# Kernel optimization log

Hardware: AMD Instinct MI355X
Metric: run time of the kernel (lower is better)

The kernel has to match this reference:

```python
import jax, jax.numpy as jnp
import numpy as np

D_MODEL = 2048
NUM_HEADS = 16
HEAD_DIM = D_MODEL // NUM_HEADS
D_FF = 4 * D_MODEL
B, L = 2, 2048
LN_EPS = 1e-6


def layer_norm(x, scale, bias):
    x32 = x.astype(jnp.float32)
    mu = jnp.mean(x32, axis=-1, keepdims=True)
    var = jnp.mean(jnp.square(x32 - mu), axis=-1, keepdims=True)
    return (x32 - mu) * jax.lax.rsqrt(var + LN_EPS) * scale + bias


def setup_inputs() -> dict:
    key = jax.random.key(0)
    ks = jax.random.split(key, 10)
    s = 1.0 / np.sqrt(D_MODEL)
    x = jax.random.normal(ks[0], (B, L, D_MODEL), dtype=jnp.float32)
    mask = jnp.tril(jnp.ones((L, L), dtype=bool))[None, None, :, :]  # causal [1,1,L,L]
    wq = jax.random.normal(ks[1], (D_MODEL, D_MODEL), jnp.float32) * s
    wk = jax.random.normal(ks[2], (D_MODEL, D_MODEL), jnp.float32) * s
    wv = jax.random.normal(ks[3], (D_MODEL, D_MODEL), jnp.float32) * s
    wo = jax.random.normal(ks[4], (D_MODEL, D_MODEL), jnp.float32) * s
    w1 = jax.random.normal(ks[5], (D_MODEL, D_FF), jnp.float32) * s
    b1 = jnp.zeros((D_FF,), jnp.float32)
    w2 = jax.random.normal(ks[6], (D_FF, D_MODEL), jnp.float32) * (1.0 / np.sqrt(D_FF))
    b2 = jnp.zeros((D_MODEL,), jnp.float32)
    ln1_scale = jnp.ones((D_MODEL,), jnp.float32)
    ln1_bias = jnp.zeros((D_MODEL,), jnp.float32)
    ln2_scale = jnp.ones((D_MODEL,), jnp.float32)
    ln2_bias = jnp.zeros((D_MODEL,), jnp.float32)
    return {"x": x, "mask": mask, "ln1_scale": ln1_scale, "ln1_bias": ln1_bias,
            "wq": wq, "wk": wk, "wv": wv, "wo": wo,
            "ln2_scale": ln2_scale, "ln2_bias": ln2_bias,
            "w1": w1, "b1": b1, "w2": w2, "b2": b2}


def reference(x, mask, ln1_scale, ln1_bias, wq, wk, wv, wo,
              ln2_scale, ln2_bias, w1, b1, w2, b2):
    residual = x
    h = layer_norm(x, ln1_scale, ln1_bias)
    b, l, _ = h.shape
    q = (h @ wq).reshape(b, l, NUM_HEADS, HEAD_DIM)
    k = (h @ wk).reshape(b, l, NUM_HEADS, HEAD_DIM)
    v = (h @ wv).reshape(b, l, NUM_HEADS, HEAD_DIM)
    scores = jnp.einsum('bqhd,bkhd->bhqk', q, k) / jnp.sqrt(jnp.float32(HEAD_DIM))
    scores = jnp.where(mask, scores, -100000.0)
    attn = jax.nn.softmax(scores, axis=-1)
    attn_out = jnp.einsum('bhqk,bkhd->bqhd', attn, v).reshape(b, l, D_MODEL)
    x = residual + attn_out @ wo
    mlp = jax.nn.gelu(layer_norm(x, ln2_scale, ln2_bias) @ w1 + b1)
    return x + mlp @ w2 + b2
```

## Files before the change

kernel.cpp:

```cpp
#include <hip/hip_runtime.h>
#include <hip/hip_bf16.h>

typedef unsigned short u16;
typedef __bf16 bf16x8 __attribute__((ext_vector_type(8)));
typedef float f32x4 __attribute__((ext_vector_type(4)));

#define D_MODEL 2048
#define D_FF    8192
#define NH      16
#define HD      128
#define BATCH   2
#define SEQ     2048
#define ROWS    (BATCH*SEQ)

__device__ __forceinline__ u16 f2bf(float f) {
  union { __hip_bfloat16 h; u16 u; } cv;
  cv.h = __float2bfloat16(f);
  return cv.u;
}

__device__ __forceinline__ void gload16(const u16* g, u16* l) {
  __builtin_amdgcn_global_load_lds((const __attribute__((address_space(1))) void*)g,
                                   (__attribute__((address_space(3))) void*)l,
                                   16, 0, 0);
}

__device__ __forceinline__ float gelu_f(float x) {
  const float k0 = 0.7978845608028654f, k1 = 0.044715f;
  return 0.5f * x * (1.0f + tanhf(k0 * (x + k1 * x * x * x)));
}

__global__ __launch_bounds__(256) void ln_bf16_kernel(
    const float* __restrict__ x, const float* __restrict__ sc,
    const float* __restrict__ bs, u16* __restrict__ out)
{
  __shared__ float red[8];
  const int row = blockIdx.x, t = threadIdx.x;
  const int w = t >> 6, l = t & 63;
  const float* xr = x + (size_t)row * D_MODEL;
  float4 a = ((const float4*)xr)[t*2];
  float4 b = ((const float4*)xr)[t*2+1];
  float s  = a.x+a.y+a.z+a.w + b.x+b.y+b.z+b.w;
  float s2 = a.x*a.x+a.y*a.y+a.z*a.z+a.w*a.w + b.x*b.x+b.y*b.y+b.z*b.z+b.w*b.w;
  for (int off = 32; off; off >>= 1) { s += __shfl_down(s, off); s2 += __shfl_down(s2, off); }
  if (l == 0) { red[w] = s; red[4+w] = s2; }
  __syncthreads();
  s  = red[0]+red[1]+red[2]+red[3];
  s2 = red[4]+red[5]+red[6]+red[7];
  const float mu  = s * (1.0f / D_MODEL);
  const float var = s2 * (1.0f / D_MODEL) - mu * mu;
  const float inv = rsqrtf(var + 1e-6f);
  float4 g0 = ((const float4*)sc)[t*2], g1 = ((const float4*)sc)[t*2+1];
  float4 q0 = ((const float4*)bs)[t*2], q1 = ((const float4*)bs)[t*2+1];
  union { u16 u[8]; uint4 v; } o;
  o.u[0] = f2bf((a.x-mu)*inv*g0.x + q0.x);
  o.u[1] = f2bf((a.y-mu)*inv*g0.y + q0.y);
  o.u[2] = f2bf((a.z-mu)*inv*g0.z + q0.z);
  o.u[3] = f2bf((a.w-mu)*inv*g0.w + q0.w);
  o.u[4] = f2bf((b.x-mu)*inv*g1.x + q1.x);
  o.u[5] = f2bf((b.y-mu)*inv*g1.y + q1.y);
  o.u[6] = f2bf((b.z-mu)*inv*g1.z + q1.z);
  o.u[7] = f2bf((b.w-mu)*inv*g1.w + q1.w);
  *(uint4*)(&out[(size_t)row * D_MODEL + t*8]) = o.v;
}

__global__ __launch_bounds__(256) void transpose_w(
    const float* __restrict__ in, u16* __restrict__ out, int R, int C)
{
  __shared__ float tile[32][33];
  const int t = threadIdx.x;
  const int c0 = blockIdx.x*32, r0 = blockIdx.y*32;
  const int col = t & 31, rb = t >> 5;
#pragma unroll
  for (int i = 0; i < 4; ++i)
    tile[rb + i*8][col] = in[(size_t)(r0 + rb + i*8)*C + c0 + col];
  __syncthreads();
#pragma unroll
  for (int i = 0; i < 4; ++i)
    out[(size_t)(c0 + rb + i*8)*R + r0 + col] = f2bf(tile[col][rb + i*8]);
}

__global__ __launch_bounds__(256) void transpose_v(
    const u16* __restrict__ qkv, u16* __restrict__ vt)
{
  __shared__ u16 tile[32][34];
  const int t = threadIdx.x;
  const int b = blockIdx.z;
  const int c0 = blockIdx.x*32, r0 = blockIdx.y*32;
  const int col = t & 31, rb = t >> 5;
  const u16* inb = qkv + (size_t)b*SEQ*3*D_MODEL + 2*D_MODEL;
#pragma unroll
  for (int i = 0; i < 4; ++i)
    tile[rb+i*8][col] = inb[(size_t)(r0+rb+i*8)*(3*D_MODEL) + c0+col];
  __syncthreads();
  u16* ob = vt + (size_t)b*SEQ*D_MODEL;
#pragma unroll
  for (int i = 0; i < 4; ++i)
    ob[(size_t)(c0+rb+i*8)*SEQ + r0+col] = tile[col][rb+i*8];
}

template<int EPI, int BNP>
__global__ __launch_bounds__(512, 1) void gemm8p(
    const u16* __restrict__ A, const u16* __restrict__ BT,
    void* __restrict__ Cout, const float* __restrict__ bias,
    const float* __restrict__ res, int N, int K, int gridN)
{
  constexpr int GB    = BNP / 128;
  constexpr int NI    = BNP / 64;
  constexpr int BHALF = BNP * 32;
  constexpr int BUFU  = 16384 + BNP * 64;
  __shared__ __align__(16) u16 lds[2 * BUFU];
  const int t = threadIdx.x;
  const int nwg = gridDim.x;
  const int wg = (int)blockIdx.x;
  const int wgid = (wg & 7) * (nwg >> 3) + (wg >> 3);
  const int bx = wgid % gridN, by = wgid / gridN;
  const int m0 = by * 256, n0 = bx * BNP;
  const int w = t >> 6, l = t & 63;
  const int wm = w >> 2, wn = w & 3;
  const int l15 = l & 15, lq = l >> 4;

  const int srow = t >> 2;
  const int c0s  = (t & 3) ^ ((srow >> 1) & 3);
  const u16* aS0 = A  + (size_t)(m0 + srow) * K + c0s * 8;
  const u16* aS1 = A  + (size_t)(m0 + 128 + srow) * K + c0s * 8;
  const u16* bS0 = BT + (size_t)(n0 + srow) * K + c0s * 8;
  const u16* bS1 = BT + (size_t)(n0 + (GB == 2 ? 128 : 0) + srow) * K + c0s * 8;

  int offA_[2][4], offB_[NI];
#pragma unroll
  for (int mq = 0; mq < 2; ++mq)
#pragma unroll
    for (int i2 = 0; i2 < 4; ++i2) {
      const int ra = wm * 128 + mq * 64 + i2 * 16 + l15;
      offA_[mq][i2] = ra * 32 + ((lq ^ ((ra >> 1) & 3)) * 8);
    }
#pragma unroll
  for (int j = 0; j < NI; ++j) {
    const int rb = wn * (BNP / 4) + j * 16 + l15;
    offB_[j] = rb * 32 + ((lq ^ ((rb >> 1) & 3)) * 8);
  }

  f32x4 acc[8][NI] = {};
  bf16x8 bfv[NI];
  const int nt = K >> 6;

#define STAGE_A(dst, Tn, kh) { \
    gload16(aS0 + (size_t)(Tn)*64 + (kh)*32, (dst) + (kh)*8192 + t*8); \
    gload16(aS1 + (size_t)(Tn)*64 + (kh)*32, (dst) + (kh)*8192 + 4096 + t*8); }
#define STAGE_B(dst, Tn, kh) { \
    gload16(bS0 + (size_t)(Tn)*64 + (kh)*32, (dst) + 16384 + (kh)*BHALF + t*8); \
    if (GB == 2) gload16(bS1 + (size_t)(Tn)*64 + (kh)*32, (dst) + 16384 + (kh)*BHALF + 4096 + t*8); }
#define VMS { if (GB == 2) { asm volatile("s_waitcnt vmcnt(4)" ::: "memory"); } \
              else        { asm volatile("s_waitcnt vmcnt(3)" ::: "memory"); } \
              __builtin_amdgcn_sched_barrier(0); }
#define VM0 { asm volatile("s_waitcnt vmcnt(0)" ::: "memory"); __builtin_amdgcn_sched_barrier(0); }
#define NOP { }

#define PHASE(bufc, MQ, KH, DOB, STAGECODE, WAITCODE) { \
    bf16x8 af_[4]; \
    _Pragma("unroll") \
    for (int i2 = 0; i2 < 4; ++i2) \
      af_[i2] = *(const bf16x8*)&(bufc)[offA_[MQ][i2] + (KH)*8192]; \
    if (DOB) { \
      _Pragma("unroll") \
      for (int j = 0; j < NI; ++j) \
        bfv[j] = *(const bf16x8*)&(bufc)[offB_[j] + 16384 + (KH)*BHALF]; \
    } \
    STAGECODE; \
    __builtin_amdgcn_s_barrier(); \
    asm volatile("s_waitcnt lgkmcnt(0)" ::: "memory"); \
    __builtin_amdgcn_sched_barrier(0); \
    __builtin_amdgcn_s_setprio(1); \
    _Pragma("unroll") \
    for (int i2 = 0; i2 < 4; ++i2) \
      _Pragma("unroll") \
      for (int j = 0; j < NI; ++j) \
        acc[(MQ)*4 + i2][j] = __builtin_amdgcn_mfma_f32_16x16x32_bf16(af_[i2], bfv[j], acc[(MQ)*4 + i2][j], 0, 0, 0); \
    __builtin_amdgcn_s_setprio(0); \
    WAITCODE; \
    __builtin_amdgcn_s_barrier(); }

  {
    u16* b0p = lds;
    STAGE_A(b0p, 0, 0); STAGE_B(b0p, 0, 0); STAGE_A(b0p, 0, 1); STAGE_B(b0p, 0, 1);
  }
  VMS;
  __builtin_amdgcn_s_barrier();

  for (int T = 0; T < nt - 1; ++T) {
    u16* bufc = &lds[(T & 1) * BUFU];
    u16* bufn = &lds[((T + 1) & 1) * BUFU];
    PHASE(bufc, 0, 0, 1, STAGE_A(bufn, T + 1, 0), NOP);
    PHASE(bufc, 1, 0, 0, STAGE_B(bufn, T + 1, 0), VMS);
    PHASE(bufc, 0, 1, 1, STAGE_A(bufn, T + 1, 1), NOP);
    PHASE(bufc, 1, 1, 0, STAGE_B(bufn, T + 1, 1), VMS);
  }
  {
    u16* bufc = &lds[((nt - 1) & 1) * BUFU];
    PHASE(bufc, 0, 0, 1, NOP, NOP);
    PHASE(bufc, 1, 0, 0, NOP, VM0);
    PHASE(bufc, 0, 1, 1, NOP, NOP);
    PHASE(bufc, 1, 1, 0, NOP, NOP);
  }
#undef PHASE
#undef STAGE_A
#undef STAGE_B
#undef VMS
#undef VM0
#undef NOP

  const int rowb = m0 + wm * 128;
  const int colb = n0 + wn * (BNP / 4);
#pragma unroll
  for (int mi = 0; mi < 8; ++mi) {
#pragma unroll
    for (int ni = 0; ni < NI; ++ni) {
      const int col = colb + ni * 16 + l15;
      const int row0 = rowb + mi * 16 + lq * 4;
      float bv = (EPI == 2 || EPI == 3) ? bias[col] : 0.f;
#pragma unroll
      for (int r = 0; r < 4; ++r) {
        const float v = acc[mi][ni][r];
        const size_t idx = (size_t)(row0 + r) * N + col;
        if (EPI == 0)      ((u16*)Cout)[idx] = f2bf(v);
        else if (EPI == 1) ((float*)Cout)[idx] = v + res[idx];
        else if (EPI == 2) ((u16*)Cout)[idx] = f2bf(gelu_f(v + bv));
        else               ((float*)Cout)[idx] = v + bv + res[idx];
      }
    }
  }
}

__global__ __launch_bounds__(256) void attn_kernel(
    const u16* __restrict__ qkv, const u16* __restrict__ vt,
    u16* __restrict__ out)
{
  __shared__ u16 Ks[64*128];
  __shared__ u16 Vs[128*64];
  __shared__ u16 Ps[4*16*64];
  const int t = threadIdx.x;
  const int pairi = blockIdx.x & 15, bh = blockIdx.x >> 4;
  const int b = bh >> 4, h = bh & 15;
  const int w = t >> 6, l = t & 63;
  const int l15 = l & 15, lq = l >> 4;
  const size_t kbase = (size_t)b*SEQ*(3*D_MODEL) + D_MODEL + h*HD;
  const size_t vbase = (size_t)(b*SEQ + h*HD) * SEQ;
  u16* pw = &Ps[w*1024];

  for (int qsel = 0; qsel < 2; ++qsel) {
    const int qt = qsel ? (31 - pairi) : pairi;

    bf16x8 qf[4];
    {
      const u16* qb = qkv + (size_t)(b*SEQ + qt*64 + w*16 + l15)*(3*D_MODEL) + h*HD;
#pragma unroll
      for (int kk = 0; kk < 4; ++kk)
        qf[kk] = *(const bf16x8*)(qb + kk*32 + lq*8);
    }
    float m[4]    = {-INFINITY, -INFINITY, -INFINITY, -INFINITY};
    float lsum[4] = {0.f, 0.f, 0.f, 0.f};
    f32x4 acc_o[8] = {};

    for (int j = 0; j <= qt; ++j) {
      __syncthreads();
#pragma unroll
      for (int i = 0; i < 4; ++i) {
        const int o16 = i*256 + t;
        {
          const int row = o16 >> 4, cs = o16 & 15;
          const int srcc = cs ^ (row & 7);
          gload16(qkv + kbase + (size_t)(j*64+row)*(3*D_MODEL) + srcc*8, &Ks[o16*8]);
        }
        {
          const int row = o16 >> 3, cs = o16 & 7;
          const int srcc = cs ^ (row & 7);
          gload16(vt + vbase + (size_t)row*SEQ + j*64 + srcc*8, &Vs[o16*8]);
        }
      }
      __syncthreads();

      f32x4 sacc[4] = {};
#pragma unroll
      for (int nf = 0; nf < 4; ++nf) {
        const int kr = nf*16 + l15;
        const int sw = kr & 7;
#pragma unroll
        for (int kk = 0; kk < 4; ++kk) {
          bf16x8 kf = *(const bf16x8*)&Ks[kr*128 + ((kk*4+lq) ^ sw)*8];
          sacc[nf] = __builtin_amdgcn_mfma_f32_16x16x32_bf16(qf[kk], kf, sacc[nf], 0, 0, 0);
        }
      }

      const float scale = 0.08838834764831845f;
      if (j == qt) {
#pragma unroll
        for (int nf = 0; nf < 4; ++nf)
#pragma unroll
          for (int r = 0; r < 4; ++r) {
            float s = sacc[nf][r] * scale;
            const int ki = nf*16 + l15;
            const int qi = w*16 + lq*4 + r;
            if (ki > qi) s = -100000.0f;
            sacc[nf][r] = s;
          }
      } else {
#pragma unroll
        for (int nf = 0; nf < 4; ++nf)
#pragma unroll
          for (int r = 0; r < 4; ++r) sacc[nf][r] *= scale;
      }

      float scal[4];
#pragma unroll
      for (int r = 0; r < 4; ++r) {
        float mx = fmaxf(fmaxf(sacc[0][r], sacc[1][r]), fmaxf(sacc[2][r], sacc[3][r]));
#pragma unroll
        for (int off = 1; off < 16; off <<= 1)
          mx = fmaxf(mx, __shfl_xor(mx, off));
        const float mn = fmaxf(m[r], mx);
        scal[r] = __expf(m[r] - mn);
        m[r] = mn;
        float rs = 0.f;
#pragma unroll
        for (int nf = 0; nf < 4; ++nf) {
          const float p = __expf(sacc[nf][r] - mn);
          sacc[nf][r] = p;
          rs += p;
        }
#pragma unroll
        for (int off = 1; off < 16; off <<= 1)
          rs += __shfl_xor(rs, off);
        lsum[r] = lsum[r]*scal[r] + rs;
      }
#pragma unroll
      for (int nf2 = 0; nf2 < 8; ++nf2)
#pragma unroll
        for (int r = 0; r < 4; ++r) acc_o[nf2][r] *= scal[r];

#pragma unroll
      for (int nf = 0; nf < 4; ++nf)
#pragma unroll
        for (int r = 0; r < 4; ++r) {
          const int qr = lq*4 + r, kc = nf*16 + l15;
          pw[qr*64 + (((kc>>3) ^ (qr&7))*8 + (kc&7))] = f2bf(sacc[nf][r]);
        }

#pragma unroll
      for (int kk2 = 0; kk2 < 2; ++kk2) {
        bf16x8 pf = *(const bf16x8*)&pw[l15*64 + (((kk2*4+lq) ^ (l15&7))*8)];
#pragma unroll
        for (int nf2 = 0; nf2 < 8; ++nf2) {
          const int vr = nf2*16 + l15;
          bf16x8 vf = *(const bf16x8*)&Vs[vr*64 + ((kk2*4+lq) ^ (vr&7))*8];
          acc_o[nf2] = __builtin_amdgcn_mfma_f32_16x16x32_bf16(pf, vf, acc_o[nf2], 0, 0, 0);
        }
      }
    }

    const size_t ro = (size_t)(b*SEQ + qt*64 + w*16 + lq*4);
#pragma unroll
    for (int r = 0; r < 4; ++r) {
      const float inv = 1.0f / lsum[r];
#pragma unroll
      for (int nf2 = 0; nf2 < 8; ++nf2)
        out[(ro + r)*D_MODEL + h*HD + nf2*16 + l15] = f2bf(acc_o[nf2][r] * inv);
    }
    __syncthreads();
  }
}

extern "C" void kernel_launch(void* const* d_in, const int* in_sizes, int n_in,
                              void* d_out, int out_size, void* d_ws, size_t ws_size,
                              hipStream_t stream)
{
  (void)in_sizes; (void)n_in; (void)out_size; (void)ws_size;
  const float* x    = (const float*)d_in[0];
  const float* ln1s = (const float*)d_in[2];
  const float* ln1b = (const float*)d_in[3];
  const float* wq   = (const float*)d_in[4];
  const float* wk   = (const float*)d_in[5];
  const float* wv   = (const float*)d_in[6];
  const float* wo   = (const float*)d_in[7];
  const float* ln2s = (const float*)d_in[8];
  const float* ln2b = (const float*)d_in[9];
  const float* w1   = (const float*)d_in[10];
  const float* b1   = (const float*)d_in[11];
  const float* w2   = (const float*)d_in[12];
  const float* b2   = (const float*)d_in[13];
  float* out = (float*)d_out;

  char* ws = (char*)d_ws;
  constexpr size_t OFF_WQKV = 0;
  constexpr size_t OFF_WO   = OFF_WQKV + (size_t)3*D_MODEL*D_MODEL*2;
  constexpr size_t OFF_W1   = OFF_WO   + (size_t)D_MODEL*D_MODEL*2;
  constexpr size_t OFF_W2   = OFF_W1   + (size_t)D_FF*D_MODEL*2;
  constexpr size_t OFF_H    = OFF_W2   + (size_t)D_MODEL*D_FF*2;
  constexpr size_t OFF_QKV  = OFF_H    + (size_t)ROWS*D_MODEL*2;
  constexpr size_t OFF_VT   = OFF_QKV  + (size_t)ROWS*3*D_MODEL*2;
  constexpr size_t OFF_ATTN = OFF_VT   + (size_t)ROWS*D_MODEL*2;
  constexpr size_t OFF_X2   = OFF_ATTN + (size_t)ROWS*D_MODEL*2;

  u16*   wqkv_bt = (u16*)(ws + OFF_WQKV);
  u16*   wo_bt   = (u16*)(ws + OFF_WO);
  u16*   w1_bt   = (u16*)(ws + OFF_W1);
  u16*   w2_bt   = (u16*)(ws + OFF_W2);
  u16*   h_bf    = (u16*)(ws + OFF_H);
  u16*   qkv     = (u16*)(ws + OFF_QKV);
  u16*   vt      = (u16*)(ws + OFF_VT);
  u16*   act     = qkv;
  u16*   attn    = (u16*)(ws + OFF_ATTN);
  float* x2      = (float*)(ws + OFF_X2);

  const dim3 B256(256), B512(512);

  transpose_w<<<dim3(64,64),  B256, 0, stream>>>(wq, wqkv_bt,                 D_MODEL, D_MODEL);
  transpose_w<<<dim3(64,64),  B256, 0, stream>>>(wk, wqkv_bt + (size_t)D_MODEL*D_MODEL,   D_MODEL, D_MODEL);
  transpose_w<<<dim3(64,64),  B256, 0, stream>>>(wv, wqkv_bt + (size_t)2*D_MODEL*D_MODEL, D_MODEL, D_MODEL);
  transpose_w<<<dim3(64,64),  B256, 0, stream>>>(wo, wo_bt, D_MODEL, D_MODEL);
  transpose_w<<<dim3(256,64), B256, 0, stream>>>(w1, w1_bt, D_MODEL, D_FF);
  transpose_w<<<dim3(64,256), B256, 0, stream>>>(w2, w2_bt, D_FF, D_MODEL);

  ln_bf16_kernel<<<ROWS, B256, 0, stream>>>(x, ln1s, ln1b, h_bf);
  gemm8p<0,128><<<dim3(768), B512, 0, stream>>>(h_bf, wqkv_bt, qkv, nullptr, nullptr, 3*D_MODEL, D_MODEL, 48);
  transpose_v<<<dim3(64,64,2), B256, 0, stream>>>(qkv, vt);
  attn_kernel<<<dim3(BATCH*NH*16), B256, 0, stream>>>(qkv, vt, attn);
  gemm8p<1,128><<<dim3(256), B512, 0, stream>>>(attn, wo_bt, (void*)x2, nullptr, x, D_MODEL, D_MODEL, 16);
  ln_bf16_kernel<<<ROWS, B256, 0, stream>>>(x2, ln2s, ln2b, h_bf);
  gemm8p<2,256><<<dim3(512), B512, 0, stream>>>(h_bf, w1_bt, act, b1, nullptr, D_FF, D_MODEL, 32);
  gemm8p<3,128><<<dim3(256), B512, 0, stream>>>(act, w2_bt, (void*)out, b2, x2, D_MODEL, D_FF, 16);
}
```

Before: 668.4 us.

## Retile GEMM warp layout and merge A/B staging into two phases per K-tile

Changes the per-wave tile mapping so each wave always covers 64 columns, using a 4x2 wave grid (64 rows per wave) when BNP is 128 instead of 2x4 with 32 columns. The four phases per K-tile become two, each loading all A and B fragments and staging A and B together. This cuts barrier count and per-wave B fragment reloads, and gives the BNP=128 case a squarer per-wave tile. The cost is that larger bursts of global loads are issued per phase, and waiting on vmcnt every phase may expose memory latency.

```diff
diff --git a/kernel.cpp b/kernel.cpp
--- a/kernel.cpp
+++ b/kernel.cpp
@@ -106,7 +106,7 @@
     const float* __restrict__ res, int N, int K, int gridN)
 {
   constexpr int GB    = BNP / 128;
-  constexpr int NI    = BNP / 64;
+  constexpr int MF    = (BNP == 256) ? 8 : 4;
   constexpr int BHALF = BNP * 32;
   constexpr int BUFU  = 16384 + BNP * 64;
   __shared__ __align__(16) u16 lds[2 * BUFU];
@@ -117,7 +117,8 @@
   const int bx = wgid % gridN, by = wgid / gridN;
   const int m0 = by * 256, n0 = bx * BNP;
   const int w = t >> 6, l = t & 63;
-  const int wm = w >> 2, wn = w & 3;
+  const int wm = (BNP == 256) ? (w >> 2) : (w >> 1);
+  const int wn = (BNP == 256) ? (w & 3) : (w & 1);
   const int l15 = l & 15, lq = l >> 4;
 
   const int srow = t >> 2;
@@ -127,28 +128,24 @@
   const u16* bS0 = BT + (size_t)(n0 + srow) * K + c0s * 8;
   const u16* bS1 = BT + (size_t)(n0 + (GB == 2 ? 128 : 0) + srow) * K + c0s * 8;
 
-  int offA_[2][4], offB_[NI];
-#pragma unroll
-  for (int mq = 0; mq < 2; ++mq)
-#pragma unroll
-    for (int i2 = 0; i2 < 4; ++i2) {
-      const int ra = wm * 128 + mq * 64 + i2 * 16 + l15;
-      offA_[mq][i2] = ra * 32 + ((lq ^ ((ra >> 1) & 3)) * 8);
-    }
-#pragma unroll
-  for (int j = 0; j < NI; ++j) {
-    const int rb = wn * (BNP / 4) + j * 16 + l15;
+  int offA_[MF], offB_[4];
+#pragma unroll
+  for (int i = 0; i < MF; ++i) {
+    const int ra = wm * (MF * 16) + i * 16 + l15;
+    offA_[i] = ra * 32 + ((lq ^ ((ra >> 1) & 3)) * 8);
+  }
+#pragma unroll
+  for (int j = 0; j < 4; ++j) {
+    const int rb = wn * 64 + j * 16 + l15;
     offB_[j] = rb * 32 + ((lq ^ ((rb >> 1) & 3)) * 8);
   }
 
-  f32x4 acc[8][NI] = {};
-  bf16x8 bfv[NI];
+  f32x4 acc[MF][4] = {};
   const int nt = K >> 6;
 
-#define STAGE_A(dst, Tn, kh) { \
+#define STAGE(dst, Tn, kh) { \
     gload16(aS0 + (size_t)(Tn)*64 + (kh)*32, (dst) + (kh)*8192 + t*8); \
-    gload16(aS1 + (size_t)(Tn)*64 + (kh)*32, (dst) + (kh)*8192 + 4096 + t*8); }
-#define STAGE_B(dst, Tn, kh) { \
+    gload16(aS1 + (size_t)(Tn)*64 + (kh)*32, (dst) + (kh)*8192 + 4096 + t*8); \
     gload16(bS0 + (size_t)(Tn)*64 + (kh)*32, (dst) + 16384 + (kh)*BHALF + t*8); \
     if (GB == 2) gload16(bS1 + (size_t)(Tn)*64 + (kh)*32, (dst) + 16384 + (kh)*BHALF + 4096 + t*8); }
 #define VMS { if (GB == 2) { asm volatile("s_waitcnt vmcnt(4)" ::: "memory"); } \
@@ -157,65 +154,55 @@
 #define VM0 { asm volatile("s_waitcnt vmcnt(0)" ::: "memory"); __builtin_amdgcn_sched_barrier(0); }
 #define NOP { }
 
-#define PHASE(bufc, MQ, KH, DOB, STAGECODE, WAITCODE) { \
-    bf16x8 af_[4]; \
+#define PHASE(bufc, KH, STAGECODE, WAITCODE) { \
+    bf16x8 af_[MF], bfv[4]; \
     _Pragma("unroll") \
-    for (int i2 = 0; i2 < 4; ++i2) \
-      af_[i2] = *(const bf16x8*)&(bufc)[offA_[MQ][i2] + (KH)*8192]; \
-    if (DOB) { \
-      _Pragma("unroll") \
-      for (int j = 0; j < NI; ++j) \
-        bfv[j] = *(const bf16x8*)&(bufc)[offB_[j] + 16384 + (KH)*BHALF]; \
-    } \
+    for (int i = 0; i < MF; ++i) \
+      af_[i] = *(const bf16x8*)&(bufc)[offA_[i] + (KH)*8192]; \
+    _Pragma("unroll") \
+    for (int j = 0; j < 4; ++j) \
+      bfv[j] = *(const bf16x8*)&(bufc)[offB_[j] + 16384 + (KH)*BHALF]; \
     STAGECODE; \
     __builtin_amdgcn_s_barrier(); \
     asm volatile("s_waitcnt lgkmcnt(0)" ::: "memory"); \
     __builtin_amdgcn_sched_barrier(0); \
     __builtin_amdgcn_s_setprio(1); \
     _Pragma("unroll") \
-    for (int i2 = 0; i2 < 4; ++i2) \
+    for (int i = 0; i < MF; ++i) \
       _Pragma("unroll") \
-      for (int j = 0; j < NI; ++j) \
-        acc[(MQ)*4 + i2][j] = __builtin_amdgcn_mfma_f32_16x16x32_bf16(af_[i2], bfv[j], acc[(MQ)*4 + i2][j], 0, 0, 0); \
+      for (int j = 0; j < 4; ++j) \
+        acc[i][j] = __builtin_amdgcn_mfma_f32_16x16x32_bf16(af_[i], bfv[j], acc[i][j], 0, 0, 0); \
     __builtin_amdgcn_s_setprio(0); \
     WAITCODE; \
     __builtin_amdgcn_s_barrier(); }
 
-  {
-    u16* b0p = lds;
-    STAGE_A(b0p, 0, 0); STAGE_B(b0p, 0, 0); STAGE_A(b0p, 0, 1); STAGE_B(b0p, 0, 1);
-  }
+  STAGE(lds, 0, 0); STAGE(lds, 0, 1);
   VMS;
   __builtin_amdgcn_s_barrier();
 
   for (int T = 0; T < nt - 1; ++T) {
     u16* bufc = &lds[(T & 1) * BUFU];
     u16* bufn = &lds[((T + 1) & 1) * BUFU];
-    PHASE(bufc, 0, 0, 1, STAGE_A(bufn, T + 1, 0), NOP);
-    PHASE(bufc, 1, 0, 0, STAGE_B(bufn, T + 1, 0), VMS);
-    PHASE(bufc, 0, 1, 1, STAGE_A(bufn, T + 1, 1), NOP);
-    PHASE(bufc, 1, 1, 0, STAGE_B(bufn, T + 1, 1), VMS);
+    PHASE(bufc, 0, STAGE(bufn, T + 1, 0), VMS);
+    PHASE(bufc, 1, STAGE(bufn, T + 1, 1), VMS);
   }
   {
     u16* bufc = &lds[((nt - 1) & 1) * BUFU];
-    PHASE(bufc, 0, 0, 1, NOP, NOP);
-    PHASE(bufc, 1, 0, 0, NOP, VM0);
-    PHASE(bufc, 0, 1, 1, NOP, NOP);
-    PHASE(bufc, 1, 1, 0, NOP, NOP);
+    PHASE(bufc, 0, NOP, VM0);
+    PHASE(bufc, 1, NOP, NOP);
   }
 #undef PHASE
-#undef STAGE_A
-#undef STAGE_B
+#undef STAGE
 #undef VMS
 #undef VM0
 #undef NOP
 
-  const int rowb = m0 + wm * 128;
-  const int colb = n0 + wn * (BNP / 4);
-#pragma unroll
-  for (int mi = 0; mi < 8; ++mi) {
-#pragma unroll
-    for (int ni = 0; ni < NI; ++ni) {
+  const int rowb = m0 + wm * (MF * 16);
+  const int colb = n0 + wn * 64;
+#pragma unroll
+  for (int mi = 0; mi < MF; ++mi) {
+#pragma unroll
+    for (int ni = 0; ni < 4; ++ni) {
       const int col = colb + ni * 16 + l15;
       const int row0 = rowb + mi * 16 + lq * 4;
       float bv = (EPI == 2 || EPI == 3) ? bias[col] : 0.f;
```

Result: no change. 671.8 us (+0.5%).

## Double-buffer K/V tiles in attention and vectorize weight transpose

Applied to the files above, without the earlier changes.

The attention kernel now keeps two LDS buffers for the K and V tiles and issues the async loads for tile j+1 before computing on tile j. This hides global-load latency behind the MFMA work and replaces the two __syncthreads per iteration with a single waitcnt plus barrier. Separately, the weight transpose moves to 64x64 tiles with float4 loads and ushort4 stores to cut memory transactions. Doubling the K/V buffers raises LDS use per block, which may reduce occupancy.

```diff
diff --git a/kernel.cpp b/kernel.cpp
--- a/kernel.cpp
+++ b/kernel.cpp
@@ -67,17 +67,25 @@
 __global__ __launch_bounds__(256) void transpose_w(
     const float* __restrict__ in, u16* __restrict__ out, int R, int C)
 {
-  __shared__ float tile[32][33];
+  __shared__ float tile[64][65];
   const int t = threadIdx.x;
-  const int c0 = blockIdx.x*32, r0 = blockIdx.y*32;
-  const int col = t & 31, rb = t >> 5;
-#pragma unroll
-  for (int i = 0; i < 4; ++i)
-    tile[rb + i*8][col] = in[(size_t)(r0 + rb + i*8)*C + c0 + col];
+  const int c0 = blockIdx.x*64, r0 = blockIdx.y*64;
+  const int cq = (t & 15) * 4, rb = t >> 4;
+#pragma unroll
+  for (int i = 0; i < 4; ++i) {
+    const float4 v = *(const float4*)&in[(size_t)(r0 + rb + i*16)*C + c0 + cq];
+    tile[rb + i*16][cq+0] = v.x; tile[rb + i*16][cq+1] = v.y;
+    tile[rb + i*16][cq+2] = v.z; tile[rb + i*16][cq+3] = v.w;
+  }
   __syncthreads();
 #pragma unroll
-  for (int i = 0; i < 4; ++i)
-    out[(size_t)(c0 + rb + i*8)*R + r0 + col] = f2bf(tile[col][rb + i*8]);
+  for (int i = 0; i < 4; ++i) {
+    const int oc = rb + i*16;
+    ushort4 o;
+    o.x = f2bf(tile[cq+0][oc]); o.y = f2bf(tile[cq+1][oc]);
+    o.z = f2bf(tile[cq+2][oc]); o.w = f2bf(tile[cq+3][oc]);
+    *(ushort4*)&out[(size_t)(c0 + oc)*R + r0 + cq] = o;
+  }
 }
 
 __global__ __launch_bounds__(256) void transpose_v(
@@ -236,8 +244,8 @@
     const u16* __restrict__ qkv, const u16* __restrict__ vt,
     u16* __restrict__ out)
 {
-  __shared__ u16 Ks[64*128];
-  __shared__ u16 Vs[128*64];
+  __shared__ u16 Ks[2][64*128];
+  __shared__ u16 Vs[2][128*64];
   __shared__ u16 Ps[4*16*64];
   const int t = threadIdx.x;
   const int pairi = blockIdx.x & 15, bh = blockIdx.x >> 4;
@@ -248,6 +256,18 @@
   const size_t vbase = (size_t)(b*SEQ + h*HD) * SEQ;
   u16* pw = &Ps[w*1024];
 
+#define STAGEKV(j, bi) { \
+    _Pragma("unroll") \
+    for (int i = 0; i < 4; ++i) { \
+      const int o16 = i*256 + t; \
+      { const int row = o16 >> 4, cs = o16 & 15; \
+        const int srcc = cs ^ (row & 7); \
+        gload16(qkv + kbase + (size_t)((j)*64+row)*(3*D_MODEL) + srcc*8, &Ks[bi][o16*8]); } \
+      { const int row = o16 >> 3, cs = o16 & 7; \
+        const int srcc = cs ^ (row & 7); \
+        gload16(vt + vbase + (size_t)row*SEQ + (j)*64 + srcc*8, &Vs[bi][o16*8]); } \
+    } }
+
   for (int qsel = 0; qsel < 2; ++qsel) {
     const int qt = qsel ? (31 - pairi) : pairi;
 
@@ -262,23 +282,14 @@
     float lsum[4] = {0.f, 0.f, 0.f, 0.f};
     f32x4 acc_o[8] = {};
 
+    STAGEKV(0, 0);
+    asm volatile("s_waitcnt vmcnt(0)" ::: "memory");
+    __builtin_amdgcn_sched_barrier(0);
+    __builtin_amdgcn_s_barrier();
+
     for (int j = 0; j <= qt; ++j) {
-      __syncthreads();
-#pragma unroll
-      for (int i = 0; i < 4; ++i) {
-        const int o16 = i*256 + t;
-        {
-          const int row = o16 >> 4, cs = o16 & 15;
-          const int srcc = cs ^ (row & 7);
-          gload16(qkv + kbase + (size_t)(j*64+row)*(3*D_MODEL) + srcc*8, &Ks[o16*8]);
-        }
-        {
-          const int row = o16 >> 3, cs = o16 & 7;
-          const int srcc = cs ^ (row & 7);
-          gload16(vt + vbase + (size_t)row*SEQ + j*64 + srcc*8, &Vs[o16*8]);
-        }
-      }
-      __syncthreads();
+      const int bi = j & 1;
+      if (j < qt) STAGEKV(j + 1, bi ^ 1);
 
       f32x4 sacc[4] = {};
 #pragma unroll
@@ -287,7 +298,7 @@
         const int sw = kr & 7;
 #pragma unroll
         for (int kk = 0; kk < 4; ++kk) {
-          bf16x8 kf = *(const bf16x8*)&Ks[kr*128 + ((kk*4+lq) ^ sw)*8];
+          bf16x8 kf = *(const bf16x8*)&Ks[bi][kr*128 + ((kk*4+lq) ^ sw)*8];
           sacc[nf] = __builtin_amdgcn_mfma_f32_16x16x32_bf16(qf[kk], kf, sacc[nf], 0, 0, 0);
         }
       }
@@ -352,10 +363,14 @@
 #pragma unroll
         for (int nf2 = 0; nf2 < 8; ++nf2) {
           const int vr = nf2*16 + l15;
-          bf16x8 vf = *(const bf16x8*)&Vs[vr*64 + ((kk2*4+lq) ^ (vr&7))*8];
+          bf16x8 vf = *(const bf16x8*)&Vs[bi][vr*64 + ((kk2*4+lq) ^ (vr&7))*8];
           acc_o[nf2] = __builtin_amdgcn_mfma_f32_16x16x32_bf16(pf, vf, acc_o[nf2], 0, 0, 0);
         }
       }
+
+      asm volatile("s_waitcnt vmcnt(0)" ::: "memory");
+      __builtin_amdgcn_sched_barrier(0);
+      __builtin_amdgcn_s_barrier();
     }
 
     const size_t ro = (size_t)(b*SEQ + qt*64 + w*16 + lq*4);
@@ -366,8 +381,8 @@
       for (int nf2 = 0; nf2 < 8; ++nf2)
         out[(ro + r)*D_MODEL + h*HD + nf2*16 + l15] = f2bf(acc_o[nf2][r] * inv);
     }
-    __syncthreads();
-  }
+  }
+#undef STAGEKV
 }
 
 extern "C" void kernel_launch(void* const* d_in, const int* in_sizes, int n_in,
@@ -414,12 +429,12 @@
 
   const dim3 B256(256), B512(512);
 
-  transpose_w<<<dim3(64,64),  B256, 0, stream>>>(wq, wqkv_bt,                 D_MODEL, D_MODEL);
-  transpose_w<<<dim3(64,64),  B256, 0, stream>>>(wk, wqkv_bt + (size_t)D_MODEL*D_MODEL,   D_MODEL, D_MODEL);
-  transpose_w<<<dim3(64,64),  B256, 0, stream>>>(wv, wqkv_bt + (size_t)2*D_MODEL*D_MODEL, D_MODEL, D_MODEL);
-  transpose_w<<<dim3(64,64),  B256, 0, stream>>>(wo, wo_bt, D_MODEL, D_MODEL);
-  transpose_w<<<dim3(256,64), B256, 0, stream>>>(w1, w1_bt, D_MODEL, D_FF);
-  transpose_w<<<dim3(64,256), B256, 0, stream>>>(w2, w2_bt, D_FF, D_MODEL);
+  transpose_w<<<dim3(32,32),  B256, 0, stream>>>(wq, wqkv_bt,                 D_MODEL, D_MODEL);
+  transpose_w<<<dim3(32,32),  B256, 0, stream>>>(wk, wqkv_bt + (size_t)D_MODEL*D_MODEL,   D_MODEL, D_MODEL);
+  transpose_w<<<dim3(32,32),  B256, 0, stream>>>(wv, wqkv_bt + (size_t)2*D_MODEL*D_MODEL, D_MODEL, D_MODEL);
+  transpose_w<<<dim3(32,32),  B256, 0, stream>>>(wo, wo_bt, D_MODEL, D_MODEL);
+  transpose_w<<<dim3(128,32), B256, 0, stream>>>(w1, w1_bt, D_MODEL, D_FF);
+  transpose_w<<<dim3(32,128), B256, 0, stream>>>(w2, w2_bt, D_FF, D_MODEL);
 
   ln_bf16_kernel<<<ROWS, B256, 0, stream>>>(x, ln1s, ln1b, h_bf);
   gemm8p<0,128><<<dim3(768), B512, 0, stream>>>(h_bf, wqkv_bt, qkv, nullptr, nullptr, 3*D_MODEL, D_MODEL, 48);
```

New measurement: 728.5 us. 1.09x slower.
